# Kernel tuning notes

Measured on AMD Instinct MI355X. Metric: run time of the kernel, lower is better.

The kernel has to match this reference:

```python
import jax, jax.numpy as jnp
import numpy as np

K = 3; PAD = 1; CIN = 64; COUT = 64; B = 4; H = 128; W = 128


def setup_inputs() -> dict:
    key = jax.random.key(0)
    k1, k2, k3 = jax.random.split(key, 3)
    x = jax.random.normal(k1, (B, CIN, H, W), dtype=jnp.float32)
    # offset-predicting conv: [2*K*K, Cin, K, K]; small init -> sub-pixel offsets
    w_off = jax.random.normal(k2, (2 * K * K, CIN, K, K), dtype=jnp.float32) * 0.01
    b_off = jnp.zeros((2 * K * K,), dtype=jnp.float32)
    # deformable conv weight (bias=False): [Cout, Cin, K, K]
    w_def = jax.random.normal(k3, (COUT, CIN, K, K), dtype=jnp.float32) * 0.05
    return {"x": x, "w_off": w_off, "b_off": b_off, "w_def": w_def}


def _deform_conv(x, w_off, b_off, w_def):
    Bb, Cin, Hh, Ww = x.shape
    KK = K * K
    # 1) predict offsets with a regular 3x3 conv (stride 1, pad 1)
    off = jax.lax.conv_general_dilated(
        x, w_off, window_strides=(1, 1), padding=[(PAD, PAD), (PAD, PAD)],
        dimension_numbers=("NCHW", "OIHW", "NCHW"))
    off = off + b_off[None, :, None, None]          # [B, 2*KK, H, W]
    off = off.reshape(Bb, KK, 2, Hh, Ww)            # torchvision layout: (dy, dx) per tap
    dy, dx = off[:, :, 0], off[:, :, 1]             # [B, KK, H, W]

    # 2) sampling coordinates: p = p0 + p_k + offset
    ky = (jnp.arange(KK) // K).astype(x.dtype)
    kx = (jnp.arange(KK) % K).astype(x.dtype)
    hh = jnp.arange(Hh, dtype=x.dtype)
    ww = jnp.arange(Ww, dtype=x.dtype)
    py = hh[None, None, :, None] - PAD + ky[None, :, None, None] + dy   # [B,KK,H,W]
    px = ww[None, None, None, :] - PAD + kx[None, :, None, None] + dx

    # 3) bilinear sampling with zero padding outside the image
    y0f = jnp.floor(py); x0f = jnp.floor(px)
    fy = py - y0f; fx = px - x0f
    y0 = y0f.astype(jnp.int32); x0 = x0f.astype(jnp.int32)
    x_flat = x.reshape(Bb, Cin, Hh * Ww)

    def gather(yi, xi):
        valid = (yi >= 0) & (yi < Hh) & (xi >= 0) & (xi < Ww)
        idx = jnp.clip(yi, 0, Hh - 1) * Ww + jnp.clip(xi, 0, Ww - 1)     # [B,KK,H,W]
        g = jax.vmap(lambda xf, ix: xf[:, ix.reshape(-1)])(x_flat, idx)  # [B,Cin,KK*H*W]
        return g.reshape(Bb, Cin, KK, Hh, Ww) * valid[:, None].astype(x.dtype)

    sampled = (gather(y0, x0)         * ((1 - fy) * (1 - fx))[:, None]
             + gather(y0, x0 + 1)     * ((1 - fy) * fx)[:, None]
             + gather(y0 + 1, x0)     * (fy * (1 - fx))[:, None]
             + gather(y0 + 1, x0 + 1) * (fy * fx)[:, None])               # [B,Cin,KK,H,W]

    # 4) convolution accumulation over (Cin, kernel taps)
    return jnp.einsum('bckhw,ock->bohw', sampled, w_def.reshape(COUT, Cin, KK))


def reference(x, w_off, b_off, w_def):
    return _deform_conv(x, w_off, b_off, w_def)
```

## Files before the change

### kernel.cpp

```cpp
#include <hip/hip_runtime.h>
#include <hip/hip_fp16.h>

#define Bn   4
#define CINc 64
#define COUTc 64
#define Hn   128
#define Wn   128
#define HW   (Hn * Wn)
#define KKc  9
#define NOFF 18

typedef short bf16x8 __attribute__((ext_vector_type(8)));
typedef float f32x4  __attribute__((ext_vector_type(4)));
typedef float f32x2  __attribute__((ext_vector_type(2)));

__device__ inline unsigned short f2bf(float f) {
    unsigned int u = __float_as_uint(f);
    return (unsigned short)((u + 0x7fffu + ((u >> 16) & 1u)) >> 16);
}

__device__ inline void dma16(const void* g, void* l) {
#if __has_builtin(__builtin_amdgcn_global_load_lds)
    __builtin_amdgcn_global_load_lds(
        (__attribute__((address_space(1))) void*)(g),
        (__attribute__((address_space(3))) void*)(l), 16, 0, 0);
#else
    *(uint4*)l = *(const uint4*)g;
#endif
}

__global__ __launch_bounds__(256) void prep_all(
        const float* __restrict__ x, unsigned short* __restrict__ xt,
        const float* __restrict__ w_off, const float* __restrict__ w_def,
        unsigned short* __restrict__ wkb_sw, unsigned short* __restrict__ wob_sw) {
    int gb = blockIdx.x;
    int t  = threadIdx.x;
    if (gb < 1024) {
        __shared__ float s[64][65];
        int half = gb & 1;
        int h    = (gb >> 1) & 127;
        int b    = gb >> 8;
        int w0   = half * 64;

        const float* xb = x + (size_t)b * CINc * HW + (size_t)h * Wn + w0;
        int c0 = t >> 4, wq = (t & 15) * 4;
        #pragma unroll
        for (int i = 0; i < 4; ++i) {
            int c = c0 + i * 16;
            float4 v = *(const float4*)(xb + (size_t)c * HW + wq);
            s[c][wq]     = v.x;
            s[c][wq + 1] = v.y;
            s[c][wq + 2] = v.z;
            s[c][wq + 3] = v.w;
        }
        __syncthreads();

        int cpair = t & 31, pxg = t >> 5;
        unsigned* xtp = (unsigned*)xt;
        #pragma unroll
        for (int i = 0; i < 8; ++i) {
            int px = pxg * 8 + i;
            float v0 = s[cpair * 2][px], v1 = s[cpair * 2 + 1][px];
            unsigned d = (unsigned)f2bf(v0) | ((unsigned)f2bf(v1) << 16);
            xtp[(((size_t)(b * Hn + h) * Wn) + w0 + px) * 32 + cpair] = d;
        }
        return;
    }
    int idx = (gb - 1024) * 256 + t;
    if (idx < 36864) {
        int j = idx & 7, l = (idx >> 3) & 63, s = idx >> 9;
        int k = s >> 3, kc = (s >> 2) & 1, ot = s & 3;
        int l15 = l & 15, quad = l >> 4;
        int o = ot * 16 + l15, c = kc * 32 + quad * 8 + j;
        wkb_sw[idx] = f2bf(w_def[((size_t)o * 64 + c) * 9 + k]);
    }
    int i2 = idx - 36864;
    if (i2 >= 0 && i2 < 18432) {
        int j = i2 & 7, l = (i2 >> 3) & 63, s = i2 >> 9;
        int tt = s >> 2, kc = (s >> 1) & 1, mt = s & 1;
        int l15 = l & 15, quad = l >> 4;
        int m = mt * 16 + l15, c = kc * 32 + quad * 8 + j;
        unsigned short v = 0;
        if (m < NOFF) v = f2bf(w_off[((size_t)m * 64 + c) * 9 + tt]);
        wob_sw[i2] = v;
    }
}


#define BFBUILD(C, kc, BF, W0, W1, W2, W3)                                   \
    do {                                                                     \
        const unsigned* t0 = (const unsigned*)&(C)[(kc) * 4 + 0];            \
        const unsigned* t1 = (const unsigned*)&(C)[(kc) * 4 + 1];            \
        const unsigned* b0 = (const unsigned*)&(C)[(kc) * 4 + 2];            \
        const unsigned* b1 = (const unsigned*)&(C)[(kc) * 4 + 3];            \
        _Pragma("unroll")                                                    \
        for (int jd = 0; jd < 4; ++jd) {                                     \
            f32x2 t0p = {__uint_as_float(t0[jd] << 16),                      \
                         __uint_as_float(t0[jd] & 0xFFFF0000u)};             \
            f32x2 t1p = {__uint_as_float(t1[jd] << 16),                      \
                         __uint_as_float(t1[jd] & 0xFFFF0000u)};             \
            f32x2 b0p = {__uint_as_float(b0[jd] << 16),                      \
                         __uint_as_float(b0[jd] & 0xFFFF0000u)};             \
            f32x2 b1p = {__uint_as_float(b1[jd] << 16),                      \
                         __uint_as_float(b1[jd] & 0xFFFF0000u)};             \
            f32x2 vv = t0p * (W0) + t1p * (W1) + b0p * (W2) + b1p * (W3);    \
            unsigned pk;                                                     \
            asm("v_cvt_pk_bf16_f32 %0, %1, %2"                               \
                : "=v"(pk) : "v"(vv.x), "v"(vv.y));                          \
            (BF).u[jd] = pk;                                                 \
        }                                                                    \
    } while (0)

#define TAP(k, SOFF)                                                         \
    do {                                                                     \
        const uint4* C = R[(k) & 1];                                         \
        union { unsigned u; __half2 hv; } c01, c23;                          \
        c01.u = pw01[(k)]; c23.u = pw23[(k)];                                \
        float W0 = __low2float(c01.hv), W1 = __high2float(c01.hv);           \
        float W2 = __low2float(c23.hv), W3 = __high2float(c23.hv);           \
        union { bf16x8 v; unsigned u[4]; } bfa, bfb;                         \
        BFBUILD(C, 0, bfa, W0, W1, W2, W3);                                  \
        BFBUILD(C, 1, bfb, W0, W1, W2, W3);                                  \
        _Pragma("unroll")                                                    \
        for (int ot = 0; ot < 4; ++ot) {                                     \
            bf16x8 af0 = s_w[(((k) * 2 + 0) * 4 + ot + (SOFF)) * 64 + lane]; \
            acc[ot] = __builtin_amdgcn_mfma_f32_16x16x32_bf16(               \
                af0, bfa.v, acc[ot], 0, 0, 0);                               \
            bf16x8 af1 = s_w[(((k) * 2 + 1) * 4 + ot + (SOFF)) * 64 + lane]; \
            acc[ot] = __builtin_amdgcn_mfma_f32_16x16x32_bf16(               \
                af1, bfb.v, acc[ot], 0, 0, 0);                               \
        }                                                                    \
    } while (0)

#define FETCH(kk, st)                                                \
    do {                                                             \
        unsigned ad_ = ad[kk];                                       \
        unsigned xc_ = ad_ >> 16;                                    \
        unsigned at_ = (((ad_ & 255u) << 7) + xc_) << 6;             \
        unsigned ab_ = ((((ad_ >> 8) & 255u) << 7) + xc_) << 6;      \
        R[st][0] = *(const uint4*)(xtb + at_ + co0);                 \
        R[st][1] = *(const uint4*)(xtb + at_ + 64 + co0);            \
        R[st][2] = *(const uint4*)(xtb + ab_ + co0);                 \
        R[st][3] = *(const uint4*)(xtb + ab_ + 64 + co0);            \
        R[st][4] = *(const uint4*)(xtb + at_ + co1);                 \
        R[st][5] = *(const uint4*)(xtb + at_ + 64 + co1);            \
        R[st][6] = *(const uint4*)(xtb + ab_ + co1);                 \
        R[st][7] = *(const uint4*)(xtb + ab_ + 64 + co1);            \
    } while (0)

__global__ __launch_bounds__(256, 4) void fused_deform_v18(
        const unsigned short* __restrict__ xt,
        const unsigned short* __restrict__ wob_sw,
        const unsigned short* __restrict__ wkb_sw,
        const float* __restrict__ b_off, float* __restrict__ out) {
    __shared__ bf16x8 s_w[36 * 64];

    int gid  = blockIdx.x;
    int xcd  = gid & 7;
    int r    = gid >> 3;
    int wh   = r & 1;
    int j    = r >> 1;
    int hh   = j & 15;
    int b    = j >> 4;
    int h    = xcd * 16 + hh;
    int tid  = threadIdx.x;
    int lane = tid & 63;
    int wave = __builtin_amdgcn_readfirstlane(tid >> 6);
    int l15  = lane & 15;
    int quad = lane >> 4;
    int p    = wh * 64 + wave * 16 + l15;

    #pragma unroll
    for (int i = 0; i < 9; ++i) {
        int seg = i * 4 + wave;
        int ebase = seg * 64;
        dma16((const uint4*)wob_sw + ebase + lane,
              (char*)s_w + (size_t)ebase * 16);
    }

    uint4 L[9][2];
    unsigned msk[9];
    const unsigned short* xtb = xt + (size_t)b * HW * 64;
    #pragma unroll
    for (int t9 = 0; t9 < 9; ++t9) {
        int ty = t9 / 3, tx = t9 % 3;
        int y  = h - 1 + ty;
        int xg = p - 1 + tx;
        bool v = (y >= 0) && (y < Hn) && (xg >= 0) && (xg < Wn);
        msk[t9] = v ? 0xFFFFFFFFu : 0u;
        int yc = min(max(y, 0), Hn - 1);
        int xc = min(max(xg, 0), Wn - 1);
        size_t base = ((size_t)yc * Wn + xc) * 64;
        L[t9][0] = *(const uint4*)(xtb + base + quad * 8);
        L[t9][1] = *(const uint4*)(xtb + base + 32 + quad * 8);
    }
    __syncthreads();

    f32x4 oa0 = (f32x4){0.f, 0.f, 0.f, 0.f};
    f32x4 oa1 = (f32x4){0.f, 0.f, 0.f, 0.f};
    #pragma unroll
    for (int t9 = 0; t9 < 9; ++t9) {
        unsigned m = msk[t9];
        #pragma unroll
        for (int kc = 0; kc < 2; ++kc) {
            union { bf16x8 v; uint4 u; } bf;
            bf.u = L[t9][kc];
            bf.u.x &= m; bf.u.y &= m; bf.u.z &= m; bf.u.w &= m;
            bf16x8 a0 = s_w[((t9 * 2 + kc) * 2 + 0) * 64 + lane];
            bf16x8 a1 = s_w[((t9 * 2 + kc) * 2 + 1) * 64 + lane];
            oa0 = __builtin_amdgcn_mfma_f32_16x16x32_bf16(a0, bf.v, oa0, 0, 0, 0);
            oa1 = __builtin_amdgcn_mfma_f32_16x16x32_bf16(a1, bf.v, oa1, 0, 0, 0);
        }
    }

    unsigned my_ad[3]  = {0, 0, 0};
    unsigned my_w01[3] = {0, 0, 0};
    unsigned my_w23[3] = {0, 0, 0};
    auto phase1 = [&](int k, float dy, float dx, int slot) {
        float py  = (float)(h - 1 + k / 3) + dy;
        float pxf = (float)(p - 1 + k % 3) + dx;
        float y0f = floorf(py), x0f = floorf(pxf);
        float fy = py - y0f, fx = pxf - x0f;
        int y0 = (int)y0f, x0 = (int)x0f;
        bool vy0 = (y0 >= 0) & (y0 < Hn);
        bool vy1 = (y0 + 1 >= 0) & (y0 + 1 < Hn);
        bool vx0 = (x0 >= 0) & (x0 < Wn);
        bool vx1 = (x0 + 1 >= 0) & (x0 + 1 < Wn);
        float wy0 = vy0 ? 1.f - fy : 0.f;
        float wy1 = vy1 ? fy : 0.f;
        float wx0 = vx0 ? 1.f - fx : 0.f;
        float wx1 = vx1 ? fx : 0.f;
        int xc = min(max(x0, 0), Wn - 2);
        bool sel0 = (min(max(x0, 0), Wn - 1) != xc);
        bool sel1 = ((min(max(x0 + 1, 0), Wn - 1) - xc) == 1);
        float Wa = (sel0 ? 0.f : wx0) + (sel1 ? 0.f : wx1);
        float Wb = (sel0 ? wx0 : 0.f) + (sel1 ? wx1 : 0.f);
        int yc0 = min(max(y0, 0), Hn - 1), yc1 = min(max(y0 + 1, 0), Hn - 1);
        union { __half2 hv; unsigned u; } c01, c23;
        c01.hv = __floats2half2_rn(wy0 * Wa, wy0 * Wb);
        c23.hv = __floats2half2_rn(wy1 * Wa, wy1 * Wb);
        my_ad[slot]  = (unsigned)yc0 | ((unsigned)yc1 << 8) | ((unsigned)xc << 16);
        my_w01[slot] = c01.u;
        my_w23[slot] = c23.u;
    };
    int kb = quad * 2;
    phase1(kb,     oa0[0] + b_off[4 * quad],     oa0[1] + b_off[4 * quad + 1], 0);
    phase1(kb + 1, oa0[2] + b_off[4 * quad + 2], oa0[3] + b_off[4 * quad + 3], 1);
    if (quad == 0)
        phase1(8, oa1[0] + b_off[16], oa1[1] + b_off[17], 2);
    __syncthreads();

    #pragma unroll
    for (int i = 0; i < 8; ++i) {
        int seg = i * 4 + wave;
        dma16((const uint4*)wkb_sw + (size_t)seg * 64 + lane,
              (char*)s_w + (size_t)seg * 1024);
    }

    unsigned ad[KKc], pw01[KKc], pw23[KKc];
    #pragma unroll
    for (int k = 0; k < KKc; ++k) {
        int src  = (k < 8) ? ((k >> 1) * 16 + l15) : l15;
        int slot = (k < 8) ? (k & 1) : 2;
        ad[k]   = (unsigned)__shfl((int)my_ad[slot],  src, 64);
        pw01[k] = (unsigned)__shfl((int)my_w01[slot], src, 64);
        pw23[k] = (unsigned)__shfl((int)my_w23[slot], src, 64);
    }
    __syncthreads();

    f32x4 acc[4];
    #pragma unroll
    for (int ot = 0; ot < 4; ++ot) acc[ot] = (f32x4){0.f, 0.f, 0.f, 0.f};

    uint4 R[2][8];
    int co0 = quad * 8, co1 = 32 + quad * 8;

    FETCH(0, 0);
    FETCH(1, 1); TAP(0, 0);
    FETCH(2, 0); TAP(1, 0);
    FETCH(3, 1); TAP(2, 0);
    FETCH(4, 0); TAP(3, 0);
    __syncthreads();

    #pragma unroll
    for (int i = 0; i < 8; ++i) {
        int seg = i * 4 + wave;
        dma16((const uint4*)wkb_sw + (size_t)(32 + seg) * 64 + lane,
              (char*)s_w + (size_t)seg * 1024);
    }

    union { bf16x8 v; unsigned u[4]; } bf40, bf41;
    {
        const uint4* C = R[0];
        union { unsigned u; __half2 hv; } c01, c23;
        c01.u = pw01[4]; c23.u = pw23[4];
        float W0 = __low2float(c01.hv), W1 = __high2float(c01.hv);
        float W2 = __low2float(c23.hv), W3 = __high2float(c23.hv);
        BFBUILD(C, 0, bf40, W0, W1, W2, W3);
        BFBUILD(C, 1, bf41, W0, W1, W2, W3);
    }
    FETCH(5, 1);
    __syncthreads();

    #pragma unroll
    for (int ot = 0; ot < 4; ++ot) {
        bf16x8 af0 = s_w[(0 + ot) * 64 + lane];
        acc[ot] = __builtin_amdgcn_mfma_f32_16x16x32_bf16(af0, bf40.v, acc[ot], 0, 0, 0);
        bf16x8 af1 = s_w[(4 + ot) * 64 + lane];
        acc[ot] = __builtin_amdgcn_mfma_f32_16x16x32_bf16(af1, bf41.v, acc[ot], 0, 0, 0);
    }

    FETCH(6, 0); TAP(5, -32);
    FETCH(7, 1); TAP(6, -32);
    FETCH(8, 0); TAP(7, -32);
    __syncthreads();

    #pragma unroll
    for (int i = 0; i < 2; ++i) {
        int seg = i * 4 + wave;
        dma16((const uint4*)wkb_sw + (size_t)(64 + seg) * 64 + lane,
              (char*)s_w + (size_t)seg * 1024);
    }

    union { bf16x8 v; unsigned u[4]; } bf80, bf81;
    {
        const uint4* C = R[0];
        union { unsigned u; __half2 hv; } c01, c23;
        c01.u = pw01[8]; c23.u = pw23[8];
        float W0 = __low2float(c01.hv), W1 = __high2float(c01.hv);
        float W2 = __low2float(c23.hv), W3 = __high2float(c23.hv);
        BFBUILD(C, 0, bf80, W0, W1, W2, W3);
        BFBUILD(C, 1, bf81, W0, W1, W2, W3);
    }
    __syncthreads();

    #pragma unroll
    for (int ot = 0; ot < 4; ++ot) {
        bf16x8 af0 = s_w[(0 + ot) * 64 + lane];
        acc[ot] = __builtin_amdgcn_mfma_f32_16x16x32_bf16(af0, bf80.v, acc[ot], 0, 0, 0);
        bf16x8 af1 = s_w[(4 + ot) * 64 + lane];
        acc[ot] = __builtin_amdgcn_mfma_f32_16x16x32_bf16(af1, bf81.v, acc[ot], 0, 0, 0);
    }

    #pragma unroll
    for (int ot = 0; ot < 4; ++ot)
        #pragma unroll
        for (int rr = 0; rr < 4; ++rr) {
            int o = ot * 16 + quad * 4 + rr;
            out[(((size_t)b * COUTc + o) * Hn + h) * Wn + p] = acc[ot][rr];
        }
}

extern "C" void kernel_launch(void* const* d_in, const int* in_sizes, int n_in,
                              void* d_out, int out_size, void* d_ws, size_t ws_size,
                              hipStream_t stream) {
    const float* x     = (const float*)d_in[0];
    const float* w_off = (const float*)d_in[1];
    const float* b_off = (const float*)d_in[2];
    const float* w_def = (const float*)d_in[3];
    float* out = (float*)d_out;

    char* ws = (char*)d_ws;
    unsigned short* xt = (unsigned short*)ws;
    ws += (size_t)Bn * HW * CINc * sizeof(unsigned short);
    unsigned short* wkb_sw = (unsigned short*)ws;
    ws += 36864 * sizeof(unsigned short);
    unsigned short* wob_sw = (unsigned short*)ws;

    prep_all<<<1024 + 216, 256, 0, stream>>>(x, xt, w_off, w_def, wkb_sw, wob_sw);
    fused_deform_v18<<<Bn * Hn * 2, 256, 0, stream>>>(xt, wob_sw, wkb_sw, b_off, out);
}
```

Before: 116.9 us.

## Make deform kernel persistent with all weights resident in LDS

The fused kernel now launches 256 blocks of 512 threads. Each block loads both the offset-conv weights and all deformable-conv weights into 108 KB of dynamic LDS once, then processes two full image rows (128 pixels each) in a loop. This removes the repeated staged weight DMA and the many __syncthreads barriers between tap groups, and it spreads the weight load over two rows. In exchange the large LDS footprint limits occupancy to about one block per CU, and only 256 blocks run with 8 waves each, so latency hiding may suffer.

```diff
diff --git a/kernel.cpp b/kernel.cpp
--- a/kernel.cpp
+++ b/kernel.cpp
@@ -111,7 +111,7 @@
         }                                                                    \
     } while (0)
 
-#define TAP(k, SOFF)                                                         \
+#define TAP(k)                                                               \
     do {                                                                     \
         const uint4* C = R[(k) & 1];                                         \
         union { unsigned u; __half2 hv; } c01, c23;                          \
@@ -123,10 +123,10 @@
         BFBUILD(C, 1, bfb, W0, W1, W2, W3);                                  \
         _Pragma("unroll")                                                    \
         for (int ot = 0; ot < 4; ++ot) {                                     \
-            bf16x8 af0 = s_w[(((k) * 2 + 0) * 4 + ot + (SOFF)) * 64 + lane]; \
+            bf16x8 af0 = s_w[(((k) * 2 + 0) * 4 + ot + 36) * 64 + lane];     \
             acc[ot] = __builtin_amdgcn_mfma_f32_16x16x32_bf16(               \
                 af0, bfa.v, acc[ot], 0, 0, 0);                               \
-            bf16x8 af1 = s_w[(((k) * 2 + 1) * 4 + ot + (SOFF)) * 64 + lane]; \
+            bf16x8 af1 = s_w[(((k) * 2 + 1) * 4 + ot + 36) * 64 + lane];     \
             acc[ot] = __builtin_amdgcn_mfma_f32_16x16x32_bf16(               \
                 af1, bfb.v, acc[ot], 0, 0, 0);                               \
         }                                                                    \
@@ -148,207 +148,152 @@
         R[st][7] = *(const uint4*)(xtb + ab_ + 64 + co1);            \
     } while (0)
 
-__global__ __launch_bounds__(256, 4) void fused_deform_v18(
+__global__ __launch_bounds__(512, 2) void fused_deform_v19(
         const unsigned short* __restrict__ xt,
         const unsigned short* __restrict__ wob_sw,
         const unsigned short* __restrict__ wkb_sw,
         const float* __restrict__ b_off, float* __restrict__ out) {
-    __shared__ bf16x8 s_w[36 * 64];
+    extern __shared__ bf16x8 s_w[];
 
     int gid  = blockIdx.x;
-    int xcd  = gid & 7;
-    int r    = gid >> 3;
-    int wh   = r & 1;
-    int j    = r >> 1;
-    int hh   = j & 15;
-    int b    = j >> 4;
-    int h    = xcd * 16 + hh;
     int tid  = threadIdx.x;
     int lane = tid & 63;
     int wave = __builtin_amdgcn_readfirstlane(tid >> 6);
     int l15  = lane & 15;
     int quad = lane >> 4;
-    int p    = wh * 64 + wave * 16 + l15;
 
     #pragma unroll
-    for (int i = 0; i < 9; ++i) {
-        int seg = i * 4 + wave;
-        int ebase = seg * 64;
-        dma16((const uint4*)wob_sw + ebase + lane,
-              (char*)s_w + (size_t)ebase * 16);
-    }
-
-    uint4 L[9][2];
-    unsigned msk[9];
-    const unsigned short* xtb = xt + (size_t)b * HW * 64;
-    #pragma unroll
-    for (int t9 = 0; t9 < 9; ++t9) {
-        int ty = t9 / 3, tx = t9 % 3;
-        int y  = h - 1 + ty;
-        int xg = p - 1 + tx;
-        bool v = (y >= 0) && (y < Hn) && (xg >= 0) && (xg < Wn);
-        msk[t9] = v ? 0xFFFFFFFFu : 0u;
-        int yc = min(max(y, 0), Hn - 1);
-        int xc = min(max(xg, 0), Wn - 1);
-        size_t base = ((size_t)yc * Wn + xc) * 64;
-        L[t9][0] = *(const uint4*)(xtb + base + quad * 8);
-        L[t9][1] = *(const uint4*)(xtb + base + 32 + quad * 8);
-    }
-    __syncthreads();
-
-    f32x4 oa0 = (f32x4){0.f, 0.f, 0.f, 0.f};
-    f32x4 oa1 = (f32x4){0.f, 0.f, 0.f, 0.f};
-    #pragma unroll
-    for (int t9 = 0; t9 < 9; ++t9) {
-        unsigned m = msk[t9];
-        #pragma unroll
-        for (int kc = 0; kc < 2; ++kc) {
-            union { bf16x8 v; uint4 u; } bf;
-            bf.u = L[t9][kc];
-            bf.u.x &= m; bf.u.y &= m; bf.u.z &= m; bf.u.w &= m;
-            bf16x8 a0 = s_w[((t9 * 2 + kc) * 2 + 0) * 64 + lane];
-            bf16x8 a1 = s_w[((t9 * 2 + kc) * 2 + 1) * 64 + lane];
-            oa0 = __builtin_amdgcn_mfma_f32_16x16x32_bf16(a0, bf.v, oa0, 0, 0, 0);
-            oa1 = __builtin_amdgcn_mfma_f32_16x16x32_bf16(a1, bf.v, oa1, 0, 0, 0);
-        }
-    }
-
-    unsigned my_ad[3]  = {0, 0, 0};
-    unsigned my_w01[3] = {0, 0, 0};
-    unsigned my_w23[3] = {0, 0, 0};
-    auto phase1 = [&](int k, float dy, float dx, int slot) {
-        float py  = (float)(h - 1 + k / 3) + dy;
-        float pxf = (float)(p - 1 + k % 3) + dx;
-        float y0f = floorf(py), x0f = floorf(pxf);
-        float fy = py - y0f, fx = pxf - x0f;
-        int y0 = (int)y0f, x0 = (int)x0f;
-        bool vy0 = (y0 >= 0) & (y0 < Hn);
-        bool vy1 = (y0 + 1 >= 0) & (y0 + 1 < Hn);
-        bool vx0 = (x0 >= 0) & (x0 < Wn);
-        bool vx1 = (x0 + 1 >= 0) & (x0 + 1 < Wn);
-        float wy0 = vy0 ? 1.f - fy : 0.f;
-        float wy1 = vy1 ? fy : 0.f;
-        float wx0 = vx0 ? 1.f - fx : 0.f;
-        float wx1 = vx1 ? fx : 0.f;
-        int xc = min(max(x0, 0), Wn - 2);
-        bool sel0 = (min(max(x0, 0), Wn - 1) != xc);
-        bool sel1 = ((min(max(x0 + 1, 0), Wn - 1) - xc) == 1);
-        float Wa = (sel0 ? 0.f : wx0) + (sel1 ? 0.f : wx1);
-        float Wb = (sel0 ? wx0 : 0.f) + (sel1 ? wx1 : 0.f);
-        int yc0 = min(max(y0, 0), Hn - 1), yc1 = min(max(y0 + 1, 0), Hn - 1);
-        union { __half2 hv; unsigned u; } c01, c23;
-        c01.hv = __floats2half2_rn(wy0 * Wa, wy0 * Wb);
-        c23.hv = __floats2half2_rn(wy1 * Wa, wy1 * Wb);
-        my_ad[slot]  = (unsigned)yc0 | ((unsigned)yc1 << 8) | ((unsigned)xc << 16);
-        my_w01[slot] = c01.u;
-        my_w23[slot] = c23.u;
-    };
-    int kb = quad * 2;
-    phase1(kb,     oa0[0] + b_off[4 * quad],     oa0[1] + b_off[4 * quad + 1], 0);
-    phase1(kb + 1, oa0[2] + b_off[4 * quad + 2], oa0[3] + b_off[4 * quad + 3], 1);
-    if (quad == 0)
-        phase1(8, oa1[0] + b_off[16], oa1[1] + b_off[17], 2);
-    __syncthreads();
-
-    #pragma unroll
-    for (int i = 0; i < 8; ++i) {
-        int seg = i * 4 + wave;
-        dma16((const uint4*)wkb_sw + (size_t)seg * 64 + lane,
-              (char*)s_w + (size_t)seg * 1024);
-    }
-
-    unsigned ad[KKc], pw01[KKc], pw23[KKc];
-    #pragma unroll
-    for (int k = 0; k < KKc; ++k) {
-        int src  = (k < 8) ? ((k >> 1) * 16 + l15) : l15;
-        int slot = (k < 8) ? (k & 1) : 2;
-        ad[k]   = (unsigned)__shfl((int)my_ad[slot],  src, 64);
-        pw01[k] = (unsigned)__shfl((int)my_w01[slot], src, 64);
-        pw23[k] = (unsigned)__shfl((int)my_w23[slot], src, 64);
-    }
-    __syncthreads();
-
-    f32x4 acc[4];
-    #pragma unroll
-    for (int ot = 0; ot < 4; ++ot) acc[ot] = (f32x4){0.f, 0.f, 0.f, 0.f};
-
-    uint4 R[2][8];
-    int co0 = quad * 8, co1 = 32 + quad * 8;
-
-    FETCH(0, 0);
-    FETCH(1, 1); TAP(0, 0);
-    FETCH(2, 0); TAP(1, 0);
-    FETCH(3, 1); TAP(2, 0);
-    FETCH(4, 0); TAP(3, 0);
-    __syncthreads();
-
-    #pragma unroll
-    for (int i = 0; i < 8; ++i) {
-        int seg = i * 4 + wave;
-        dma16((const uint4*)wkb_sw + (size_t)(32 + seg) * 64 + lane,
-              (char*)s_w + (size_t)seg * 1024);
-    }
-
-    union { bf16x8 v; unsigned u[4]; } bf40, bf41;
-    {
-        const uint4* C = R[0];
-        union { unsigned u; __half2 hv; } c01, c23;
-        c01.u = pw01[4]; c23.u = pw23[4];
-        float W0 = __low2float(c01.hv), W1 = __high2float(c01.hv);
-        float W2 = __low2float(c23.hv), W3 = __high2float(c23.hv);
-        BFBUILD(C, 0, bf40, W0, W1, W2, W3);
-        BFBUILD(C, 1, bf41, W0, W1, W2, W3);
-    }
-    FETCH(5, 1);
-    __syncthreads();
-
-    #pragma unroll
-    for (int ot = 0; ot < 4; ++ot) {
-        bf16x8 af0 = s_w[(0 + ot) * 64 + lane];
-        acc[ot] = __builtin_amdgcn_mfma_f32_16x16x32_bf16(af0, bf40.v, acc[ot], 0, 0, 0);
-        bf16x8 af1 = s_w[(4 + ot) * 64 + lane];
-        acc[ot] = __builtin_amdgcn_mfma_f32_16x16x32_bf16(af1, bf41.v, acc[ot], 0, 0, 0);
-    }
-
-    FETCH(6, 0); TAP(5, -32);
-    FETCH(7, 1); TAP(6, -32);
-    FETCH(8, 0); TAP(7, -32);
-    __syncthreads();
-
-    #pragma unroll
-    for (int i = 0; i < 2; ++i) {
-        int seg = i * 4 + wave;
-        dma16((const uint4*)wkb_sw + (size_t)(64 + seg) * 64 + lane,
-              (char*)s_w + (size_t)seg * 1024);
-    }
-
-    union { bf16x8 v; unsigned u[4]; } bf80, bf81;
-    {
-        const uint4* C = R[0];
-        union { unsigned u; __half2 hv; } c01, c23;
-        c01.u = pw01[8]; c23.u = pw23[8];
-        float W0 = __low2float(c01.hv), W1 = __high2float(c01.hv);
-        float W2 = __low2float(c23.hv), W3 = __high2float(c23.hv);
-        BFBUILD(C, 0, bf80, W0, W1, W2, W3);
-        BFBUILD(C, 1, bf81, W0, W1, W2, W3);
-    }
-    __syncthreads();
-
-    #pragma unroll
-    for (int ot = 0; ot < 4; ++ot) {
-        bf16x8 af0 = s_w[(0 + ot) * 64 + lane];
-        acc[ot] = __builtin_amdgcn_mfma_f32_16x16x32_bf16(af0, bf80.v, acc[ot], 0, 0, 0);
-        bf16x8 af1 = s_w[(4 + ot) * 64 + lane];
-        acc[ot] = __builtin_amdgcn_mfma_f32_16x16x32_bf16(af1, bf81.v, acc[ot], 0, 0, 0);
-    }
-
-    #pragma unroll
-    for (int ot = 0; ot < 4; ++ot)
-        #pragma unroll
-        for (int rr = 0; rr < 4; ++rr) {
-            int o = ot * 16 + quad * 4 + rr;
-            out[(((size_t)b * COUTc + o) * Hn + h) * Wn + p] = acc[ot][rr];
-        }
+    for (int i = 0; i < 14; ++i) {
+        int seg = i * 8 + wave;
+        if (seg < 108) {
+            const uint4* src = (seg < 36)
+                ? (const uint4*)wob_sw + (size_t)seg * 64 + lane
+                : (const uint4*)wkb_sw + (size_t)(seg - 36) * 64 + lane;
+            dma16(src, (char*)s_w + (size_t)seg * 1024);
+        }
+    }
+
+    bool first = true;
+    #pragma unroll 1
+    for (int row = 0; row < 2; ++row) {
+        int gv   = gid + row * 256;
+        int xcd  = gv & 7;
+        int j    = gv >> 3;
+        int hh   = j & 15;
+        int b    = j >> 4;
+        int h    = xcd * 16 + hh;
+        int p    = wave * 16 + l15;
+
+        uint4 L[9][2];
+        unsigned msk[9];
+        const unsigned short* xtb = xt + (size_t)b * HW * 64;
+        #pragma unroll
+        for (int t9 = 0; t9 < 9; ++t9) {
+            int ty = t9 / 3, tx = t9 % 3;
+            int y  = h - 1 + ty;
+            int xg = p - 1 + tx;
+            bool v = (y >= 0) && (y < Hn) && (xg >= 0) && (xg < Wn);
+            msk[t9] = v ? 0xFFFFFFFFu : 0u;
+            int yc = min(max(y, 0), Hn - 1);
+            int xc = min(max(xg, 0), Wn - 1);
+            size_t base = ((size_t)yc * Wn + xc) * 64;
+            L[t9][0] = *(const uint4*)(xtb + base + quad * 8);
+            L[t9][1] = *(const uint4*)(xtb + base + 32 + quad * 8);
+        }
+        if (first) {
+            __syncthreads();
+            first = false;
+        }
+
+        f32x4 oa0 = (f32x4){0.f, 0.f, 0.f, 0.f};
+        f32x4 oa1 = (f32x4){0.f, 0.f, 0.f, 0.f};
+        #pragma unroll
+        for (int t9 = 0; t9 < 9; ++t9) {
+            unsigned m = msk[t9];
+            #pragma unroll
+            for (int kc = 0; kc < 2; ++kc) {
+                union { bf16x8 v; uint4 u; } bf;
+                bf.u = L[t9][kc];
+                bf.u.x &= m; bf.u.y &= m; bf.u.z &= m; bf.u.w &= m;
+                bf16x8 a0 = s_w[((t9 * 2 + kc) * 2 + 0) * 64 + lane];
+                bf16x8 a1 = s_w[((t9 * 2 + kc) * 2 + 1) * 64 + lane];
+                oa0 = __builtin_amdgcn_mfma_f32_16x16x32_bf16(a0, bf.v, oa0, 0, 0, 0);
+                oa1 = __builtin_amdgcn_mfma_f32_16x16x32_bf16(a1, bf.v, oa1, 0, 0, 0);
+            }
+        }
+
+        unsigned my_ad[3]  = {0, 0, 0};
+        unsigned my_w01[3] = {0, 0, 0};
+        unsigned my_w23[3] = {0, 0, 0};
+        auto phase1 = [&](int k, float dy, float dx, int slot) {
+            float py  = (float)(h - 1 + k / 3) + dy;
+            float pxf = (float)(p - 1 + k % 3) + dx;
+            float y0f = floorf(py), x0f = floorf(pxf);
+            float fy = py - y0f, fx = pxf - x0f;
+            int y0 = (int)y0f, x0 = (int)x0f;
+            bool vy0 = (y0 >= 0) & (y0 < Hn);
+            bool vy1 = (y0 + 1 >= 0) & (y0 + 1 < Hn);
+            bool vx0 = (x0 >= 0) & (x0 < Wn);
+            bool vx1 = (x0 + 1 >= 0) & (x0 + 1 < Wn);
+            float wy0 = vy0 ? 1.f - fy : 0.f;
+            float wy1 = vy1 ? fy : 0.f;
+            float wx0 = vx0 ? 1.f - fx : 0.f;
+            float wx1 = vx1 ? fx : 0.f;
+            int xc = min(max(x0, 0), Wn - 2);
+            bool sel0 = (min(max(x0, 0), Wn - 1) != xc);
+            bool sel1 = ((min(max(x0 + 1, 0), Wn - 1) - xc) == 1);
+            float Wa = (sel0 ? 0.f : wx0) + (sel1 ? 0.f : wx1);
+            float Wb = (sel0 ? wx0 : 0.f) + (sel1 ? wx1 : 0.f);
+            int yc0 = min(max(y0, 0), Hn - 1), yc1 = min(max(y0 + 1, 0), Hn - 1);
+            union { __half2 hv; unsigned u; } c01, c23;
+            c01.hv = __floats2half2_rn(wy0 * Wa, wy0 * Wb);
+            c23.hv = __floats2half2_rn(wy1 * Wa, wy1 * Wb);
+            my_ad[slot]  = (unsigned)yc0 | ((unsigned)yc1 << 8) | ((unsigned)xc << 16);
+            my_w01[slot] = c01.u;
+            my_w23[slot] = c23.u;
+        };
+        int kb = quad * 2;
+        phase1(kb,     oa0[0] + b_off[4 * quad],     oa0[1] + b_off[4 * quad + 1], 0);
+        phase1(kb + 1, oa0[2] + b_off[4 * quad + 2], oa0[3] + b_off[4 * quad + 3], 1);
+        if (quad == 0)
+            phase1(8, oa1[0] + b_off[16], oa1[1] + b_off[17], 2);
+
+        unsigned ad[KKc], pw01[KKc], pw23[KKc];
+        #pragma unroll
+        for (int k = 0; k < KKc; ++k) {
+            int src  = (k < 8) ? ((k >> 1) * 16 + l15) : l15;
+            int slot = (k < 8) ? (k & 1) : 2;
+            ad[k]   = (unsigned)__shfl((int)my_ad[slot],  src, 64);
+            pw01[k] = (unsigned)__shfl((int)my_w01[slot], src, 64);
+            pw23[k] = (unsigned)__shfl((int)my_w23[slot], src, 64);
+        }
+
+        f32x4 acc[4];
+        #pragma unroll
+        for (int ot = 0; ot < 4; ++ot) acc[ot] = (f32x4){0.f, 0.f, 0.f, 0.f};
+
+        uint4 R[2][8];
+        int co0 = quad * 8, co1 = 32 + quad * 8;
+
+        FETCH(0, 0);
+        FETCH(1, 1); TAP(0);
+        FETCH(2, 0); TAP(1);
+        FETCH(3, 1); TAP(2);
+        FETCH(4, 0); TAP(3);
+        FETCH(5, 1); TAP(4);
+        FETCH(6, 0); TAP(5);
+        FETCH(7, 1); TAP(6);
+        FETCH(8, 0); TAP(7);
+        TAP(8);
+
+        #pragma unroll
+        for (int ot = 0; ot < 4; ++ot)
+            #pragma unroll
+            for (int rr = 0; rr < 4; ++rr) {
+                int o = ot * 16 + quad * 4 + rr;
+                out[(((size_t)b * COUTc + o) * Hn + h) * Wn + p] = acc[ot][rr];
+            }
+    }
 }
 
 extern "C" void kernel_launch(void* const* d_in, const int* in_sizes, int n_in,
@@ -367,6 +312,14 @@
     ws += 36864 * sizeof(unsigned short);
     unsigned short* wob_sw = (unsigned short*)ws;
 
+    static bool attr_set = false;
+    if (!attr_set) {
+        (void)hipFuncSetAttribute((const void*)fused_deform_v19,
+                                  hipFuncAttributeMaxDynamicSharedMemorySize,
+                                  110592);
+        attr_set = true;
+    }
+
     prep_all<<<1024 + 216, 256, 0, stream>>>(x, xt, w_off, w_def, wkb_sw, wob_sw);
-    fused_deform_v18<<<Bn * Hn * 2, 256, 0, stream>>>(xt, wob_sw, wkb_sw, b_off, out);
-}
+    fused_deform_v19<<<256, 512, 110592, stream>>>(xt, wob_sw, wkb_sw, b_off, out);
+}
```

After: 116.5 us. No clear change (-0.4%).
